# Optimization experiments

Hardware: AMD Instinct MI355X
Metric: run time of the kernel (lower is better)

Reference implementation:

```python
import jax, jax.numpy as jnp
from jax import lax
import numpy as np

# --- module hyperparams (match S2_GaussianBlur(nr=2048, nc=2048, kernelSize=10, scale=2, RealData=False)) ---
NR, NC, KS, SCALE = 2048, 2048, 10, 2
MTF = np.array([0.38, 0.34, 0.34, 0.26, 0.22, 0.23])  # mtf[[4,5,6,8,10,11]] for scale==2
C = len(MTF)


def _gaussian_kernels():
    # sigmas = scale * sqrt(-2 ln(mtf) / pi^2)
    sigmas = SCALE * np.sqrt(-2.0 * np.log(MTF) / np.pi ** 2)  # (C,)
    end = int(KS / 2) - 0.5
    coords = np.arange(-end, end + 1.0, 1.0)  # (KS,) = [-4.5, ..., 4.5]
    g1 = np.exp(-coords[None, :] ** 2 / (2.0 * sigmas[:, None] ** 2)) / (
        sigmas[:, None] * np.sqrt(2.0 * np.pi))  # (C,KS)
    k = g1[:, :, None] * g1[:, None, :]  # separable outer product -> (C,KS,KS)
    k = k / k.sum(axis=(1, 2), keepdims=True)
    return k.astype(np.float32)


_KERNELS = jnp.asarray(_gaussian_kernels())  # (C,KS,KS), fixed buffers (requires_grad=False)

# Offsets replicating: circular pad by (nr//2, nc//2), conv with full-image kernel B
# (Gaussian patch placed at [row_start:row_end, col_start:col_end], then flipped both
# axes), crop [0:-1, 0:-1].  This collapses exactly to a circular cross-correlation
# with the flipped KSxKS patch at a fixed shift:
_MIDL, _MIDC = NR // 2, NC // 2
_EB = -int(SCALE / 2)
_ROW_START = int(_MIDL - KS / 2 + _EB)
_COL_START = int(_MIDC - KS / 2 + _EB)
_PAD_T = _MIDL + _ROW_START + KS - NR  # left/top circular pad (=4 here)
_PAD_L = _MIDC + _COL_START + KS - NC
assert 0 <= _PAD_T < KS and 0 <= _PAD_L < KS


def setup_inputs() -> dict:
    key = jax.random.key(0)
    x = jax.random.normal(key, (1, C, NR, NC), dtype=jnp.float32)
    return {"x": x}


def _blur(x):
    # circular (wrap) pad so every output pixel sees its KSxKS circular neighborhood
    xpad = jnp.pad(x, ((0, 0), (0, 0), (_PAD_T, KS - 1 - _PAD_T), (_PAD_L, KS - 1 - _PAD_L)), mode="wrap")
    # flipped Gaussian patch (the full-image kernel B was flipped on both axes)
    w = _KERNELS[:, ::-1, ::-1][:, None, :, :]  # (C,1,KS,KS), depthwise
    return lax.conv_general_dilated(
        xpad, w, window_strides=(1, 1), padding="VALID",
        dimension_numbers=("NCHW", "OIHW", "NCHW"), feature_group_count=C)


def reference(x):
    return _blur(x)  # (1,C,NR,NC)
```

## Files before the change

kernel.cpp:

```cpp
#include <hip/hip_runtime.h>
#include <math.h>

constexpr int C   = 6;
constexpr int NR  = 2048;
constexpr int NC  = 2048;
constexpr int KS  = 10;
constexpr int PAD = 4;

constexpr int R     = 32;
constexpr int NIT   = R + KS - 1;
constexpr int CPT   = 4;
constexpr int BW    = 256 * CPT;
constexpr int DEPTH = 4;
constexpr int WROW  = 272;

__device__ __constant__ float MTFf[C] = {0.38f, 0.34f, 0.34f, 0.26f, 0.22f, 0.23f};

template<int K> struct IC { static constexpr int v = K; };
template<int K, int N, typename F>
__device__ __forceinline__ void static_for(F&& f) {
    if constexpr (K < N) { f(IC<K>{}); static_for<K + 1, N>(f); }
}

template<int N> __device__ __forceinline__ void vm_wait() {
    asm volatile("s_waitcnt vmcnt(%0)" :: "n"(N) : "memory");
}

__global__ __launch_bounds__(256, 3)
void s2_blur_lds(const float* __restrict__ x, float* __restrict__ out)
{
    __shared__ __align__(16) float lds[4][DEPTH][WROW];

    const int t     = threadIdx.x;
    const int ln    = t & 63;
    const int wv    = t >> 6;
    const int c     = blockIdx.z;
    const int r0    = blockIdx.y * R;
    const int jt    = blockIdx.x * BW + t * CPT;
    const int wbase = blockIdx.x * BW + wv * 256;

    const float* xc = x   + (size_t)c * NR * NC;
    float*       oc = out + (size_t)c * NR * NC;

    float w[KS];
    {
        float mtf    = MTFf[c];
        float sig    = 2.0f * sqrtf(-2.0f * logf(mtf) / (float)(M_PI * M_PI));
        float inv2s2 = 1.0f / (2.0f * sig * sig);
        float s = 0.0f;
        #pragma unroll
        for (int d = 0; d < KS; ++d) {
            float cd = -4.5f + (float)d;
            w[d] = expf(-cd * cd * inv2s2);
            s += w[d];
        }
        #pragma unroll
        for (int d = 0; d < KS; ++d) w[d] /= s;
    }

    const int sA = (wbase -  4 + ln * 4 + NC) & (NC - 1);
    const int sB = (wbase + 12 + ln * 4 + NC) & (NC - 1);

    float* lb0 = &lds[wv][0][0];

    auto issue = [&](int k) {
        const float* rp = xc + (size_t)((r0 - PAD + k + NR) & (NR - 1)) * NC;
        float* lb = lb0 + (k & (DEPTH - 1)) * WROW;
        __builtin_amdgcn_global_load_lds(
            (const __attribute__((address_space(1))) void*)(rp + sA),
            (__attribute__((address_space(3))) void*)(lb), 16, 0, 0);
        __builtin_amdgcn_global_load_lds(
            (const __attribute__((address_space(1))) void*)(rp + sB),
            (__attribute__((address_space(3))) void*)(lb + 16), 16, 0, 0);
    };

    float acc[KS][CPT] = {};

    issue(0); issue(1); issue(2);

    static_for<0, NIT>([&](auto ic) {
        constexpr int k = decltype(ic)::v;

        if constexpr (k + 3 < NIT) issue(k + 3);

        constexpr int rem = NIT - 1 - k;
        vm_wait<2 * (rem < 3 ? rem : 3)>();

        const float* lb = lb0 + (k & (DEPTH - 1)) * WROW + ln * 4;
        float4 a0 = *(const float4*)(lb + 0);
        float4 a1 = *(const float4*)(lb + 4);
        float4 a2 = *(const float4*)(lb + 8);
        float4 a3 = *(const float4*)(lb + 12);
        const float f[16] = {a0.x, a0.y, a0.z, a0.w,
                             a1.x, a1.y, a1.z, a1.w,
                             a2.x, a2.y, a2.z, a2.w,
                             a3.x, a3.y, a3.z, a3.w};
        float H[CPT];
        #pragma unroll
        for (int q = 0; q < CPT; ++q) {
            float a = 0.0f;
            #pragma unroll
            for (int d = 0; d < KS; ++d) a = fmaf(w[d], f[q + d], a);
            H[q] = a;
        }

        #pragma unroll
        for (int o = 0; o < KS; ++o) {
            const int m = k - o;
            if (m >= 0 && m < R) {
                const int s = m % KS;
                #pragma unroll
                for (int q = 0; q < CPT; ++q)
                    acc[s][q] = fmaf(w[o], H[q], acc[s][q]);
            }
        }

        if constexpr (k >= KS - 1) {
            constexpr int m = k - (KS - 1);
            constexpr int s = m % KS;
            float* orow = oc + (size_t)(r0 + m) * NC;
            *(float4*)(orow + jt) = make_float4(acc[s][0], acc[s][1], acc[s][2], acc[s][3]);
            #pragma unroll
            for (int q = 0; q < CPT; ++q) acc[s][q] = 0.0f;
        }
    });
}

extern "C" void kernel_launch(void* const* d_in, const int* in_sizes, int n_in,
                              void* d_out, int out_size, void* d_ws, size_t ws_size,
                              hipStream_t stream) {
    const float* x = (const float*)d_in[0];
    float* out = (float*)d_out;
    dim3 grid(NC / BW, NR / R, C);
    dim3 block(256);
    s2_blur_lds<<<grid, block, 0, stream>>>(x, out);
}
```

Baseline: 184.5 us.

## Replace LDS-staged row loads with direct register-buffered global loads

Drops the global-to-LDS async staging and LDS reads. Each thread now loads four overlapping float4 vectors per input row straight into a register ring buffer, prefetched three rows ahead. This removes the LDS round trip and explicit waitcnt handling. In exchange it doubles global load instructions, relies on cache for the overlapping reads, and raises register pressure.

```diff
diff --git a/kernel.cpp b/kernel.cpp
--- a/kernel.cpp
+++ b/kernel.cpp
@@ -12,7 +12,7 @@
 constexpr int CPT   = 4;
 constexpr int BW    = 256 * CPT;
 constexpr int DEPTH = 4;
-constexpr int WROW  = 272;
+constexpr int DIST  = 3;
 
 __device__ __constant__ float MTFf[C] = {0.38f, 0.34f, 0.34f, 0.26f, 0.22f, 0.23f};
 
@@ -22,22 +22,13 @@
     if constexpr (K < N) { f(IC<K>{}); static_for<K + 1, N>(f); }
 }
 
-template<int N> __device__ __forceinline__ void vm_wait() {
-    asm volatile("s_waitcnt vmcnt(%0)" :: "n"(N) : "memory");
-}
-
 __global__ __launch_bounds__(256, 3)
-void s2_blur_lds(const float* __restrict__ x, float* __restrict__ out)
+void s2_blur_deep(const float* __restrict__ x, float* __restrict__ out)
 {
-    __shared__ __align__(16) float lds[4][DEPTH][WROW];
-
-    const int t     = threadIdx.x;
-    const int ln    = t & 63;
-    const int wv    = t >> 6;
-    const int c     = blockIdx.z;
-    const int r0    = blockIdx.y * R;
-    const int jt    = blockIdx.x * BW + t * CPT;
-    const int wbase = blockIdx.x * BW + wv * 256;
+    const int t  = threadIdx.x;
+    const int c  = blockIdx.z;
+    const int r0 = blockIdx.y * R;
+    const int jt = blockIdx.x * BW + t * CPT;
 
     const float* xc = x   + (size_t)c * NR * NC;
     float*       oc = out + (size_t)c * NR * NC;
@@ -58,43 +49,39 @@
         for (int d = 0; d < KS; ++d) w[d] /= s;
     }
 
-    const int sA = (wbase -  4 + ln * 4 + NC) & (NC - 1);
-    const int sB = (wbase + 12 + ln * 4 + NC) & (NC - 1);
+    const int off0 = (jt - PAD +  0 + NC) & (NC - 1);
+    const int off1 = (jt - PAD +  4 + NC) & (NC - 1);
+    const int off2 = (jt - PAD +  8 + NC) & (NC - 1);
+    const int off3 = (jt - PAD + 12 + NC) & (NC - 1);
 
-    float* lb0 = &lds[wv][0][0];
-
-    auto issue = [&](int k) {
-        const float* rp = xc + (size_t)((r0 - PAD + k + NR) & (NR - 1)) * NC;
-        float* lb = lb0 + (k & (DEPTH - 1)) * WROW;
-        __builtin_amdgcn_global_load_lds(
-            (const __attribute__((address_space(1))) void*)(rp + sA),
-            (__attribute__((address_space(3))) void*)(lb), 16, 0, 0);
-        __builtin_amdgcn_global_load_lds(
-            (const __attribute__((address_space(1))) void*)(rp + sB),
-            (__attribute__((address_space(3))) void*)(lb + 16), 16, 0, 0);
+    auto load_row = [&](int krow, float4& d0, float4& d1, float4& d2, float4& d3) {
+        const float* rp = xc + (size_t)((r0 - PAD + krow + NR) & (NR - 1)) * NC;
+        d0 = *(const float4*)(rp + off0);
+        d1 = *(const float4*)(rp + off1);
+        d2 = *(const float4*)(rp + off2);
+        d3 = *(const float4*)(rp + off3);
     };
 
     float acc[KS][CPT] = {};
 
-    issue(0); issue(1); issue(2);
+    float4 buf[DEPTH][4];
+    load_row(0, buf[0][0], buf[0][1], buf[0][2], buf[0][3]);
+    load_row(1, buf[1][0], buf[1][1], buf[1][2], buf[1][3]);
+    load_row(2, buf[2][0], buf[2][1], buf[2][2], buf[2][3]);
 
     static_for<0, NIT>([&](auto ic) {
         constexpr int k = decltype(ic)::v;
 
-        if constexpr (k + 3 < NIT) issue(k + 3);
+        if constexpr (k + DIST < NIT) {
+            constexpr int sl = (k + DIST) % DEPTH;
+            load_row(k + DIST, buf[sl][0], buf[sl][1], buf[sl][2], buf[sl][3]);
+        }
 
-        constexpr int rem = NIT - 1 - k;
-        vm_wait<2 * (rem < 3 ? rem : 3)>();
-
-        const float* lb = lb0 + (k & (DEPTH - 1)) * WROW + ln * 4;
-        float4 a0 = *(const float4*)(lb + 0);
-        float4 a1 = *(const float4*)(lb + 4);
-        float4 a2 = *(const float4*)(lb + 8);
-        float4 a3 = *(const float4*)(lb + 12);
-        const float f[16] = {a0.x, a0.y, a0.z, a0.w,
-                             a1.x, a1.y, a1.z, a1.w,
-                             a2.x, a2.y, a2.z, a2.w,
-                             a3.x, a3.y, a3.z, a3.w};
+        constexpr int s0 = k % DEPTH;
+        const float f[16] = {buf[s0][0].x, buf[s0][0].y, buf[s0][0].z, buf[s0][0].w,
+                             buf[s0][1].x, buf[s0][1].y, buf[s0][1].z, buf[s0][1].w,
+                             buf[s0][2].x, buf[s0][2].y, buf[s0][2].z, buf[s0][2].w,
+                             buf[s0][3].x, buf[s0][3].y, buf[s0][3].z, buf[s0][3].w};
         float H[CPT];
         #pragma unroll
         for (int q = 0; q < CPT; ++q) {
@@ -117,11 +104,11 @@
 
         if constexpr (k >= KS - 1) {
             constexpr int m = k - (KS - 1);
-            constexpr int s = m % KS;
+            constexpr int sl = m % KS;
             float* orow = oc + (size_t)(r0 + m) * NC;
-            *(float4*)(orow + jt) = make_float4(acc[s][0], acc[s][1], acc[s][2], acc[s][3]);
+            *(float4*)(orow + jt) = make_float4(acc[sl][0], acc[sl][1], acc[sl][2], acc[sl][3]);
             #pragma unroll
-            for (int q = 0; q < CPT; ++q) acc[s][q] = 0.0f;
+            for (int q = 0; q < CPT; ++q) acc[sl][q] = 0.0f;
         }
     });
 }
@@ -133,5 +120,5 @@
     float* out = (float*)d_out;
     dim3 grid(NC / BW, NR / R, C);
     dim3 block(256);
-    s2_blur_lds<<<grid, block, 0, stream>>>(x, out);
+    s2_blur_deep<<<grid, block, 0, stream>>>(x, out);
 }
```

Result: slower. 197.2 us (+6.9%).

## Deduplicate row loads with register-staged halo and double-buffered LDS

Applied to the files above, without the earlier changes.

Replaces the two overlapping async global-to-LDS loads per lane (which fetched most of each row twice) with one float4 main load per lane plus three halo loads from lanes 0-2. Rows are staged through registers and written into a two-slot per-wave LDS buffer, so the explicit vmcnt waits are dropped and the compiler places the waits. The aim is to halve the global/L2 load traffic per row. In exchange, prefetch depth falls from three rows to about two, the loads go through registers instead of async LDS DMA, and a few lanes diverge for the halo loads.

```diff
diff --git a/kernel.cpp b/kernel.cpp
--- a/kernel.cpp
+++ b/kernel.cpp
@@ -7,12 +7,11 @@
 constexpr int KS  = 10;
 constexpr int PAD = 4;
 
-constexpr int R     = 32;
-constexpr int NIT   = R + KS - 1;
-constexpr int CPT   = 4;
-constexpr int BW    = 256 * CPT;
-constexpr int DEPTH = 4;
-constexpr int WROW  = 272;
+constexpr int R    = 32;
+constexpr int NIT  = R + KS - 1;
+constexpr int CPT  = 4;
+constexpr int BW   = 256 * CPT;
+constexpr int WBUF = 272;
 
 __device__ __constant__ float MTFf[C] = {0.38f, 0.34f, 0.34f, 0.26f, 0.22f, 0.23f};
 
@@ -22,14 +21,10 @@
     if constexpr (K < N) { f(IC<K>{}); static_for<K + 1, N>(f); }
 }
 
-template<int N> __device__ __forceinline__ void vm_wait() {
-    asm volatile("s_waitcnt vmcnt(%0)" :: "n"(N) : "memory");
-}
-
 __global__ __launch_bounds__(256, 3)
-void s2_blur_lds(const float* __restrict__ x, float* __restrict__ out)
+void s2_blur_dedup(const float* __restrict__ x, float* __restrict__ out)
 {
-    __shared__ __align__(16) float lds[4][DEPTH][WROW];
+    __shared__ __align__(16) float lds[4][2][WBUF];
 
     const int t     = threadIdx.x;
     const int ln    = t & 63;
@@ -37,7 +32,7 @@
     const int c     = blockIdx.z;
     const int r0    = blockIdx.y * R;
     const int jt    = blockIdx.x * BW + t * CPT;
-    const int wbase = blockIdx.x * BW + wv * 256;
+    const int wseg  = blockIdx.x * BW + wv * 256;
 
     const float* xc = x   + (size_t)c * NR * NC;
     float*       oc = out + (size_t)c * NR * NC;
@@ -58,35 +53,43 @@
         for (int d = 0; d < KS; ++d) w[d] /= s;
     }
 
-    const int sA = (wbase -  4 + ln * 4 + NC) & (NC - 1);
-    const int sB = (wbase + 12 + ln * 4 + NC) & (NC - 1);
+    const int sMain = wseg + 4 * ln;
+    const int hidx  = (ln == 1 ? 260 : (ln == 2 ? 264 : 0));
+    const int hcol  = (wseg - 4 + hidx + NC) & (NC - 1);
 
-    float* lb0 = &lds[wv][0][0];
-
-    auto issue = [&](int k) {
-        const float* rp = xc + (size_t)((r0 - PAD + k + NR) & (NR - 1)) * NC;
-        float* lb = lb0 + (k & (DEPTH - 1)) * WROW;
-        __builtin_amdgcn_global_load_lds(
-            (const __attribute__((address_space(1))) void*)(rp + sA),
-            (__attribute__((address_space(3))) void*)(lb), 16, 0, 0);
-        __builtin_amdgcn_global_load_lds(
-            (const __attribute__((address_space(1))) void*)(rp + sB),
-            (__attribute__((address_space(3))) void*)(lb + 16), 16, 0, 0);
+    auto row_ptr = [&](int k) {
+        return xc + (size_t)((r0 - PAD + k + NR) & (NR - 1)) * NC;
+    };
+    auto load_row = [&](int k, float4& m, float4& h) {
+        const float* rp = row_ptr(k);
+        m = *(const float4*)(rp + sMain);
+        if (ln < 3) h = *(const float4*)(rp + hcol);
+    };
+    auto write_row = [&](int buf, const float4& m, const float4& h) {
+        *(float4*)(&lds[wv][buf][4 + 4 * ln]) = m;
+        if (ln < 3) *(float4*)(&lds[wv][buf][hidx]) = h;
     };
 
     float acc[KS][CPT] = {};
 
-    issue(0); issue(1); issue(2);
+    float4 mA = {}, hA = {}, mB = {}, hB = {};
+    load_row(0, mA, hA);
+    load_row(1, mB, hB);
+    write_row(0, mA, hA);
 
     static_for<0, NIT>([&](auto ic) {
         constexpr int k = decltype(ic)::v;
 
-        if constexpr (k + 3 < NIT) issue(k + 3);
+        if constexpr (k + 2 < NIT) {
+            if constexpr (k % 2 == 0) load_row(k + 2, mA, hA);
+            else                      load_row(k + 2, mB, hB);
+        }
+        if constexpr (k + 1 < NIT) {
+            if constexpr ((k + 1) % 2 == 0) write_row((k + 1) & 1, mA, hA);
+            else                            write_row((k + 1) & 1, mB, hB);
+        }
 
-        constexpr int rem = NIT - 1 - k;
-        vm_wait<2 * (rem < 3 ? rem : 3)>();
-
-        const float* lb = lb0 + (k & (DEPTH - 1)) * WROW + ln * 4;
+        const float* lb = &lds[wv][k & 1][4 * ln];
         float4 a0 = *(const float4*)(lb + 0);
         float4 a1 = *(const float4*)(lb + 4);
         float4 a2 = *(const float4*)(lb + 8);
@@ -116,12 +119,12 @@
         }
 
         if constexpr (k >= KS - 1) {
-            constexpr int m = k - (KS - 1);
-            constexpr int s = m % KS;
+            constexpr int m  = k - (KS - 1);
+            constexpr int sl = m % KS;
             float* orow = oc + (size_t)(r0 + m) * NC;
-            *(float4*)(orow + jt) = make_float4(acc[s][0], acc[s][1], acc[s][2], acc[s][3]);
+            *(float4*)(orow + jt) = make_float4(acc[sl][0], acc[sl][1], acc[sl][2], acc[sl][3]);
             #pragma unroll
-            for (int q = 0; q < CPT; ++q) acc[s][q] = 0.0f;
+            for (int q = 0; q < CPT; ++q) acc[sl][q] = 0.0f;
         }
     });
 }
@@ -133,5 +136,5 @@
     float* out = (float*)d_out;
     dim3 grid(NC / BW, NR / R, C);
     dim3 block(256);
-    s2_blur_lds<<<grid, block, 0, stream>>>(x, out);
+    s2_blur_dedup<<<grid, block, 0, stream>>>(x, out);
 }
```

New measurement: 213.9 us. 15.9% more time.
